# Kernel tuning notes

Measured on AMD Instinct MI355X. Metric: run time of the kernel, lower is better.

The kernel has to match this reference:

```python
import jax, jax.numpy as jnp
import numpy as np

INV_COEFF = 25.0
VAR_COEFF = 25.0
COV_COEFF = 1.0


def _cdist(a, b):
    # Euclidean pairwise distance, (B,N,C)x(B,M,C)->(B,N,M)
    a2 = jnp.sum(a * a, axis=-1)[:, :, None]
    b2 = jnp.sum(b * b, axis=-1)[:, None, :]
    d2 = a2 + b2 - 2.0 * jnp.einsum('bnc,bmc->bnm', a, b)
    return jnp.sqrt(jnp.maximum(d2, 0.0))


def _nn_match(input_maps, candidate_maps, distances, num_matches):
    # top-1 NN per input row, then keep the num_matches rows with the
    # smallest NN-distance, preserving original row order (matches the
    # torch sort/sort/mask + masked_select logic exactly).
    min_vals = jnp.min(distances, axis=-1)       # (B, N)
    nn_idx = jnp.argmin(distances, axis=-1)      # (B, N)
    order = jnp.argsort(min_vals, axis=1)[:, :num_matches]   # rows with smallest min-dist
    indices_selected = jnp.sort(order, axis=1)               # restore original order (B, M)
    nn_selected = jnp.take_along_axis(nn_idx, indices_selected, axis=1)  # (B, M)
    filt_in = jnp.take_along_axis(input_maps, indices_selected[..., None], axis=1)
    filt_cand = jnp.take_along_axis(candidate_maps, nn_selected[..., None], axis=1)
    return filt_in, filt_cand


def _vicreg_loss(x, y):
    # x, y: (B, M, C)
    B = x.shape[0]
    C = x.shape[-1]
    repr_loss = INV_COEFF * jnp.mean((x - y) ** 2)
    # gather_center: subtract batch mean (single-device equivalent)
    xc = x - jnp.mean(x, axis=0, keepdims=True)
    yc = y - jnp.mean(y, axis=0, keepdims=True)
    std_x = jnp.sqrt(jnp.var(xc, axis=0, ddof=1) + 1e-4)
    std_y = jnp.sqrt(jnp.var(yc, axis=0, ddof=1) + 1e-4)
    std_loss = VAR_COEFF * (jnp.mean(jax.nn.relu(1.0 - std_x)) / 2
                            + jnp.mean(jax.nn.relu(1.0 - std_y)) / 2)
    # covariance per location: permute to (M, B, C), center over batch
    xp = jnp.transpose(xc, (1, 0, 2))
    yp = jnp.transpose(yc, (1, 0, 2))
    xp = xp - jnp.mean(xp, axis=-2, keepdims=True)
    yp = yp - jnp.mean(yp, axis=-2, keepdims=True)
    cov_x = jnp.einsum('mnc,mnd->mcd', xp, xp) / (B - 1)
    cov_y = jnp.einsum('mnc,mnd->mcd', yp, yp) / (B - 1)
    off = 1.0 - jnp.eye(C, dtype=x.dtype)
    cov_loss = (jnp.sum((cov_x * off) ** 2, axis=(-2, -1)) / C / 2
                + jnp.sum((cov_y * off) ** 2, axis=(-2, -1)) / C / 2)
    cov_loss = COV_COEFF * jnp.mean(cov_loss)
    return repr_loss, std_loss, cov_loss


def _local_loss(maps_1, maps_2, location_1, location_2, num_matches):
    # L2-feature-space NN matching, both directions
    m1f_l2, m1nn_l2 = _nn_match(maps_1, maps_2, _cdist(maps_1, maps_2), num_matches)
    m2f_l2, m2nn_l2 = _nn_match(maps_2, maps_1, _cdist(maps_2, maps_1), num_matches)
    # location-space NN matching, both directions
    loc1 = location_1.reshape(location_1.shape[0], -1, location_1.shape[-1])
    loc2 = location_2.reshape(location_2.shape[0], -1, location_2.shape[-1])
    m1f_loc, m1nn_loc = _nn_match(maps_1, maps_2, _cdist(loc1, loc2), num_matches)
    m2f_loc, m2nn_loc = _nn_match(maps_2, maps_1, _cdist(loc2, loc1), num_matches)
    inv = var = cov = 0.0
    for a, b in ((m1f_l2, m1nn_l2), (m2f_l2, m2nn_l2),
                 (m1f_loc, m1nn_loc), (m2f_loc, m2nn_loc)):
        i, v, c = _vicreg_loss(a, b)
        inv = inv + i
        var = var + v
        cov = cov + c
    return inv + var + cov


def setup_inputs() -> dict:
    key = jax.random.key(0)
    k1, k2, k3, k4 = jax.random.split(key, 4)
    B, HW, C, H = 64, 784, 512, 28
    return {
        'maps_1': jax.random.normal(k1, (B, HW, C), dtype=jnp.float32),
        'maps_2': jax.random.normal(k2, (B, HW, C), dtype=jnp.float32),
        'location_1': jax.random.uniform(k3, (B, H, H, 2), dtype=jnp.float32),
        'location_2': jax.random.uniform(k4, (B, H, H, 2), dtype=jnp.float32),
        'num_matches': 256,
    }


def reference(maps_1, maps_2, location_1, location_2, num_matches):
    return _local_loss(maps_1, maps_2, location_1, location_2, num_matches)
```

## Files before the change

### kernel.cpp

```cpp
#include <hip/hip_runtime.h>
#include <stdint.h>

#define B 64
#define N 784
#define C 512
#define M 256

typedef unsigned long long u64;
typedef unsigned short u16;
typedef __attribute__((ext_vector_type(8))) short short8;
typedef __attribute__((ext_vector_type(4))) float f32x4;

static __device__ __forceinline__ u64 umin64(u64 a, u64 b) { return a < b ? a : b; }

static __device__ __forceinline__ u16 f2bf(float x) {
    unsigned u = __float_as_uint(x);
    return (u16)((u + 0x7FFFu + ((u >> 16) & 1u)) >> 16);
}
static __device__ __forceinline__ float b2f(u16 v) {
    return __uint_as_float((unsigned)v << 16);
}

static __device__ __forceinline__ void gload_lds16(const u16* g, u16* l) {
    __builtin_amdgcn_global_load_lds((const __attribute__((address_space(1))) void*)g,
                                     (__attribute__((address_space(3))) void*)l, 16, 0, 0);
}

__global__ __launch_bounds__(256) void convnorm_kernel(
    const float* __restrict__ m1, const float* __restrict__ m2,
    u16* __restrict__ abf, u16* __restrict__ bbf, float* __restrict__ nrm) {
    int w = blockIdx.x * 4 + (threadIdx.x >> 6);
    int lane = threadIdx.x & 63;
    if (w >= 2 * B * N) return;
    const float* src = (w < B * N) ? m1 : m2;
    u16* dst = (w < B * N) ? abf : bbf;
    int row = (w < B * N) ? w : w - B * N;
    const float4* p = (const float4*)(src + (size_t)row * C);
    u64* q = (u64*)(dst + (size_t)row * C);
    float s = 0.f;
#pragma unroll
    for (int i = 0; i < 2; ++i) {
        int idx = lane + i * 64;
        float4 v = p[idx];
        s += v.x * v.x + v.y * v.y + v.z * v.z + v.w * v.w;
        q[idx] = (u64)f2bf(v.x) | ((u64)f2bf(v.y) << 16) |
                 ((u64)f2bf(v.z) << 32) | ((u64)f2bf(v.w) << 48);
    }
#pragma unroll
    for (int off = 32; off > 0; off >>= 1) s += __shfl_down(s, off, 64);
    if (lane == 0) nrm[w] = s;
}

__global__ __launch_bounds__(256, 2) void feat_mfma_kernel(
    const u16* __restrict__ abf, const u16* __restrict__ bbf,
    const float* __restrict__ nrm, u64* __restrict__ rowkey) {
    int id = blockIdx.x;
    int xcd = id & 7;
    int q = id >> 3;
    int hi = q / 49, t49 = q - hi * 49;
    int b = hi * 8 + xcd;
    int tn = t49 / 7, tm = t49 - tn * 7;

    const int t = threadIdx.x;
    const int lane = t & 63, wv = t >> 6;
    const int wr = wv >> 1, wc = wv & 1;

    __shared__ __align__(16) u16 SM[2][2][128 * 64];
    __shared__ float sNa[128], sNb[128];

    const int row0 = tn * 128, col0 = tm * 128;
    if (t < 128) {
        int n = row0 + t;
        sNa[t] = (n < N) ? nrm[b * N + n] : __builtin_inff();
    } else {
        int m = col0 + (t - 128);
        sNb[t - 128] = (m < N) ? nrm[B * N + b * N + m] : __builtin_inff();
    }

    size_t aofs[4], bofs[4];
    int ldso[4];
#pragma unroll
    for (int s = 0; s < 4; ++s) {
        int c = (wv * 4 + s) * 64 + lane;
        int rl = c >> 3;
        int grp = (c & 7) ^ (rl & 7);
        int ga = row0 + rl; if (ga > N - 1) ga = N - 1;
        int gb = col0 + rl; if (gb > N - 1) gb = N - 1;
        aofs[s] = ((size_t)b * N + ga) * C + grp * 8;
        bofs[s] = ((size_t)b * N + gb) * C + grp * 8;
        ldso[s] = (wv * 4 + s) * 512;
    }

    f32x4 acc[4][4];
#pragma unroll
    for (int i = 0; i < 4; ++i)
#pragma unroll
        for (int j = 0; j < 4; ++j) acc[i][j] = (f32x4){0.f, 0.f, 0.f, 0.f};

#pragma unroll
    for (int s = 0; s < 4; ++s) {
        gload_lds16(abf + aofs[s], &SM[0][0][ldso[s]]);
        gload_lds16(bbf + bofs[s], &SM[0][1][ldso[s]]);
    }
    __syncthreads();

    for (int kt = 0; kt < 8; ++kt) {
        const int cur = kt & 1;
        if (kt < 7) {
            int ke = (kt + 1) * 64;
#pragma unroll
            for (int s = 0; s < 4; ++s) {
                gload_lds16(abf + aofs[s] + ke, &SM[cur ^ 1][0][ldso[s]]);
                gload_lds16(bbf + bofs[s] + ke, &SM[cur ^ 1][1][ldso[s]]);
            }
        }
        const u16* Als = SM[cur][0];
        const u16* Bls = SM[cur][1];
#pragma unroll
        for (int ks = 0; ks < 2; ++ks) {
            short8 afr[4], bfr[4];
            int cb = ks * 4 + (lane >> 4);
#pragma unroll
            for (int f = 0; f < 4; ++f) {
                int ra = wr * 64 + f * 16 + (lane & 15);
                afr[f] = *(const short8*)&Als[ra * 64 + ((cb ^ (ra & 7)) << 3)];
                int rb = wc * 64 + f * 16 + (lane & 15);
                bfr[f] = *(const short8*)&Bls[rb * 64 + ((cb ^ (rb & 7)) << 3)];
            }
#pragma unroll
            for (int fi = 0; fi < 4; ++fi)
#pragma unroll
                for (int fj = 0; fj < 4; ++fj)
                    acc[fi][fj] = __builtin_amdgcn_mfma_f32_16x16x32_bf16(
                        afr[fi], bfr[fj], acc[fi][fj], 0, 0, 0);
        }
        __syncthreads();
    }

    const int g4 = (lane >> 4) << 2;
    float na4[4][4], nb4[4];
#pragma unroll
    for (int fi = 0; fi < 4; ++fi) {
        float4 v = *(const float4*)&sNa[wr * 64 + fi * 16 + g4];
        na4[fi][0] = v.x; na4[fi][1] = v.y; na4[fi][2] = v.z; na4[fi][3] = v.w;
    }
#pragma unroll
    for (int fj = 0; fj < 4; ++fj) nb4[fj] = sNb[wc * 64 + fj * 16 + (lane & 15)];

    u64(*red)[33] = (u64(*)[33])SM;
    u64 ck[4] = {~0ull, ~0ull, ~0ull, ~0ull};
#pragma unroll
    for (int fi = 0; fi < 4; ++fi) {
        int rl = wr * 64 + fi * 16 + g4;
        u64 rk[4] = {~0ull, ~0ull, ~0ull, ~0ull};
#pragma unroll
        for (int fj = 0; fj < 4; ++fj) {
            unsigned colidx = (unsigned)(col0 + wc * 64 + fj * 16 + (lane & 15));
#pragma unroll
            for (int reg = 0; reg < 4; ++reg) {
                float d2 = fmaxf(na4[fi][reg] + nb4[fj] - 2.f * acc[fi][fj][reg], 0.f);
                u64 hv = ((u64)__float_as_uint(d2) << 32);
                rk[reg] = umin64(rk[reg], hv | colidx);
                ck[fj] = umin64(ck[fj], hv | (unsigned)(row0 + rl + reg));
            }
        }
#pragma unroll
        for (int reg = 0; reg < 4; ++reg)
            red[rl + reg][(wc << 4) | (lane & 15)] = rk[reg];
    }
#pragma unroll
    for (int fj = 0; fj < 4; ++fj) {
        u64 best = ck[fj];
        best = umin64(best, __shfl_xor(best, 16, 64));
        best = umin64(best, __shfl_xor(best, 32, 64));
        if (lane < 16) {
            int m = col0 + wc * 64 + fj * 16 + lane;
            if (m < N) atomicMin(&rowkey[(size_t)B * N + (size_t)b * N + m], best);
        }
    }
    __syncthreads();
    if (t < 128) {
        u64 best = red[t][0];
#pragma unroll
        for (int x = 1; x < 32; ++x) best = umin64(best, red[t][x]);
        int n = row0 + t;
        if (n < N) atomicMin(&rowkey[(size_t)b * N + n], best);
    }
}

__global__ __launch_bounds__(256) void loc_dist_kernel(
    const float* __restrict__ l1, const float* __restrict__ l2,
    u64* __restrict__ rowkey) {
    const int dir = blockIdx.z;
    const int b = blockIdx.y;
    const int t = threadIdx.x;
    const int n = blockIdx.x * 256 + t;
    __shared__ __align__(16) float4 s4[N];
    const float* Ap = dir ? l2 : l1;
    const float* Bp = dir ? l1 : l2;
    for (int i = t; i < N; i += 256) {
        float2 qv = ((const float2*)Bp)[b * N + i];
        s4[i] = make_float4(qv.x, qv.y, qv.x * qv.x + qv.y * qv.y, 0.f);
    }
    __syncthreads();
    if (n >= N) return;
    float2 a = ((const float2*)Ap)[b * N + n];
    float a2 = a.x * a.x + a.y * a.y;
    float nax = -2.f * a.x, nay = -2.f * a.y;
    u64 best = ~0ull;
#pragma unroll 4
    for (int mm = 0; mm < N; ++mm) {
        float4 v = s4[mm];
        float d2 = fmaxf(fmaf(nax, v.x, fmaf(nay, v.y, a2 + v.z)), 0.f);
        u64 kv = ((u64)__float_as_uint(d2) << 32) | (unsigned)mm;
        best = kv < best ? kv : best;
    }
    rowkey[(size_t)(2 + dir) * B * N + (size_t)b * N + n] = best;
}

__global__ __launch_bounds__(256) void select_kernel(
    const u64* __restrict__ rowkey, int* __restrict__ sel_idx,
    int* __restrict__ nn_idx) {
    const int b = blockIdx.x;
    const int dir = blockIdx.y;
    const int t = threadIdx.x;
    __shared__ u64 sk[1024];
    const u64* rk = rowkey + (size_t)dir * B * N + (size_t)b * N;
    for (int i = t; i < 1024; i += 256)
        sk[i] = (i < N) ? ((rk[i] & 0xFFFFFFFF00000000ull) | (unsigned)i) : ~0ull;
    __syncthreads();
    for (unsigned k = 2; k <= 1024; k <<= 1) {
        for (unsigned j = k >> 1; j > 0; j >>= 1) {
            for (unsigned i = t; i < 1024; i += 256) {
                unsigned ixj = i ^ j;
                if (ixj > i) {
                    u64 x = sk[i], y = sk[ixj];
                    bool up = ((i & k) == 0);
                    if ((x > y) == up) { sk[i] = y; sk[ixj] = x; }
                }
            }
            __syncthreads();
        }
    }
    unsigned myidx = (unsigned)(sk[t] & 0xFFFFFFFFull);
    __syncthreads();
    unsigned* si = (unsigned*)sk;
    si[t] = myidx;
    __syncthreads();
    for (unsigned k = 2; k <= 256; k <<= 1) {
        for (unsigned j = k >> 1; j > 0; j >>= 1) {
            unsigned i = t, ixj = i ^ j;
            if (ixj > i) {
                unsigned x = si[i], y = si[ixj];
                bool up = ((i & k) == 0);
                if ((x > y) == up) { si[i] = y; si[ixj] = x; }
            }
            __syncthreads();
        }
    }
    int sel = (int)si[t];
    sel_idx[((size_t)dir * B + b) * M + t] = sel;
    nn_idx[((size_t)dir * B + b) * M + t] = (int)(unsigned)(rk[sel] & 0xFFFFFFFFull);
}

__global__ __launch_bounds__(256, 2) void vicreg_mfma_kernel(
    const u16* __restrict__ abf, const u16* __restrict__ bbf,
    const int* __restrict__ sel_idx, const int* __restrict__ nn_idx,
    float* __restrict__ acc) {
    const int mloc = blockIdx.x;
    const int p = blockIdx.y;
    const int t = threadIdx.x;
    const int l = t & 63, w = t >> 6;

    __shared__ __align__(16) u16 Xs[2][64 * 128];
    __shared__ __align__(16) u16 Ys[2][64 * 128];
    __shared__ float colpart[4][4][128];
    __shared__ float Rsx[64], Rsy[64];
    __shared__ int xi[64], yi[64];
    __shared__ float redsc[4][4];

    if (t < 64) xi[t] = sel_idx[((size_t)p * B + t) * M + mloc];
    else if (t < 128) yi[t - 64] = nn_idx[((size_t)p * B + (t - 64)) * M + mloc];
    __syncthreads();

    const u16* Xg = (p & 1) ? bbf : abf;
    const u16* Yg = (p & 1) ? abf : bbf;
    unsigned xofs[4], yofs[4];
    int ldst[4];
#pragma unroll
    for (int s = 0; s < 4; ++s) {
        int r = w * 16 + s * 4 + (l >> 4);
        int cs = (l & 15) ^ (r & 15);
        xofs[s] = (unsigned)((r * N + xi[r]) * C + cs * 8);
        yofs[s] = (unsigned)((r * N + yi[r]) * C + cs * 8);
        ldst[s] = (w * 16 + s * 4) * 128;
    }

    f32x4 Gx[4], Gy[4], Z;
#pragma unroll
    for (int j = 0; j < 4; ++j) { Gx[j] = (f32x4){0,0,0,0}; Gy[j] = (f32x4){0,0,0,0}; }
    Z = (f32x4){0, 0, 0, 0};
    float stdacc = 0.f, covdacc = 0.f, reprp = 0.f;

#pragma unroll
    for (int s = 0; s < 4; ++s) {
        gload_lds16(Xg + xofs[s], &Xs[0][ldst[s]]);
        gload_lds16(Yg + yofs[s], &Ys[0][ldst[s]]);
    }
    __syncthreads();

    for (int kc = 0; kc < 4; ++kc) {
        const int cur = kc & 1;
        if (kc < 3) {
            int ke = (kc + 1) * 128;
#pragma unroll
            for (int s = 0; s < 4; ++s) {
                gload_lds16(Xg + xofs[s] + ke, &Xs[cur ^ 1][ldst[s]]);
                gload_lds16(Yg + yofs[s] + ke, &Ys[cur ^ 1][ldst[s]]);
            }
        }
        const u16* Xc = Xs[cur];
        const u16* Yc = Ys[cur];

#pragma unroll
        for (int ks = 0; ks < 4; ++ks) {
            int cb = ks * 4 + (l >> 4);
            int pe = (cb ^ (l & 15)) << 3;
            short8 ax = *(const short8*)&Xc[((w << 4) + (l & 15)) * 128 + pe];
            short8 ay = *(const short8*)&Yc[((w << 4) + (l & 15)) * 128 + pe];
            short8 bx[4], by[4];
#pragma unroll
            for (int j = 0; j < 4; ++j) {
                bx[j] = *(const short8*)&Xc[(j * 16 + (l & 15)) * 128 + pe];
                by[j] = *(const short8*)&Yc[(j * 16 + (l & 15)) * 128 + pe];
            }
#pragma unroll
            for (int j = 0; j < 4; ++j) {
                Gx[j] = __builtin_amdgcn_mfma_f32_16x16x32_bf16(ax, bx[j], Gx[j], 0, 0, 0);
                Gy[j] = __builtin_amdgcn_mfma_f32_16x16x32_bf16(ay, by[j], Gy[j], 0, 0, 0);
            }
            Z = __builtin_amdgcn_mfma_f32_16x16x32_bf16(ax, ay, Z, 0, 0, 0);
        }

        {
            int c4 = (l & 31) << 2;
            int cc = c4 >> 3, h = (c4 >> 2) & 1;
            int g2 = (w << 1) + (l >> 5);
            float s1x0 = 0, s1x1 = 0, s1x2 = 0, s1x3 = 0;
            float s2x0 = 0, s2x1 = 0, s2x2 = 0, s2x3 = 0;
            float s1y0 = 0, s1y1 = 0, s1y2 = 0, s1y3 = 0;
            float s2y0 = 0, s2y1 = 0, s2y2 = 0, s2y3 = 0;
#pragma unroll
            for (int rr = 0; rr < 8; ++rr) {
                int r = g2 * 8 + rr;
                int off = r * 128 + ((cc ^ (r & 15)) << 3) + h * 4;
                ushort4 vx = *(const ushort4*)&Xc[off];
                ushort4 vy = *(const ushort4*)&Yc[off];
                float x0 = b2f(vx.x), x1 = b2f(vx.y), x2 = b2f(vx.z), x3 = b2f(vx.w);
                float y0 = b2f(vy.x), y1 = b2f(vy.y), y2 = b2f(vy.z), y3 = b2f(vy.w);
                s1x0 += x0; s1x1 += x1; s1x2 += x2; s1x3 += x3;
                s2x0 = fmaf(x0, x0, s2x0); s2x1 = fmaf(x1, x1, s2x1);
                s2x2 = fmaf(x2, x2, s2x2); s2x3 = fmaf(x3, x3, s2x3);
                s1y0 += y0; s1y1 += y1; s1y2 += y2; s1y3 += y3;
                s2y0 = fmaf(y0, y0, s2y0); s2y1 = fmaf(y1, y1, s2y1);
                s2y2 = fmaf(y2, y2, s2y2); s2y3 = fmaf(y3, y3, s2y3);
            }
            s1x0 += __shfl_xor(s1x0, 32, 64); s1x1 += __shfl_xor(s1x1, 32, 64);
            s1x2 += __shfl_xor(s1x2, 32, 64); s1x3 += __shfl_xor(s1x3, 32, 64);
            s2x0 += __shfl_xor(s2x0, 32, 64); s2x1 += __shfl_xor(s2x1, 32, 64);
            s2x2 += __shfl_xor(s2x2, 32, 64); s2x3 += __shfl_xor(s2x3, 32, 64);
            s1y0 += __shfl_xor(s1y0, 32, 64); s1y1 += __shfl_xor(s1y1, 32, 64);
            s1y2 += __shfl_xor(s1y2, 32, 64); s1y3 += __shfl_xor(s1y3, 32, 64);
            s2y0 += __shfl_xor(s2y0, 32, 64); s2y1 += __shfl_xor(s2y1, 32, 64);
            s2y2 += __shfl_xor(s2y2, 32, 64); s2y3 += __shfl_xor(s2y3, 32, 64);
            if (l < 32) {
                *(float4*)&colpart[w][0][c4] = make_float4(s1x0, s1x1, s1x2, s1x3);
                *(float4*)&colpart[w][1][c4] = make_float4(s2x0, s2x1, s2x2, s2x3);
                *(float4*)&colpart[w][2][c4] = make_float4(s1y0, s1y1, s1y2, s1y3);
                *(float4*)&colpart[w][3][c4] = make_float4(s2y0, s2y1, s2y2, s2y3);
            }
        }
        __syncthreads();

        if (t < 128) {
            float s1x = 0, s2x = 0, s1y = 0, s2y = 0;
#pragma unroll
            for (int ww = 0; ww < 4; ++ww) {
                s1x += colpart[ww][0][t]; s2x += colpart[ww][1][t];
                s1y += colpart[ww][2][t]; s2y += colpart[ww][3][t];
            }
            float sx = s2x - s1x * s1x * (1.f / 64.f);
            float sy = s2y - s1y * s1y * (1.f / 64.f);
            stdacc += fmaxf(0.f, 1.f - sqrtf(sx * (1.f / 63.f) + 1e-4f)) +
                      fmaxf(0.f, 1.f - sqrtf(sy * (1.f / 63.f) + 1e-4f));
            covdacc += sx * sx + sy * sy;
            reprp += s2x + s2y;
        }
        __syncthreads();
    }

    float zd = 0.f;
    {
        int rbase = (l >> 4) << 2, col = l & 15;
#pragma unroll
        for (int reg = 0; reg < 4; ++reg)
            zd += (col == rbase + reg) ? Z[reg] : 0.f;
    }
    float rsx[4], rsy[4];
#pragma unroll
    for (int reg = 0; reg < 4; ++reg) {
        rsx[reg] = Gx[0][reg] + Gx[1][reg] + Gx[2][reg] + Gx[3][reg];
        rsy[reg] = Gy[0][reg] + Gy[1][reg] + Gy[2][reg] + Gy[3][reg];
    }
#pragma unroll
    for (int off = 1; off < 16; off <<= 1)
#pragma unroll
        for (int reg = 0; reg < 4; ++reg) {
            rsx[reg] += __shfl_xor(rsx[reg], off, 64);
            rsy[reg] += __shfl_xor(rsy[reg], off, 64);
        }
    if ((l & 15) == 0) {
#pragma unroll
        for (int reg = 0; reg < 4; ++reg) {
            Rsx[(w << 4) + ((l >> 4) << 2) + reg] = rsx[reg];
            Rsy[(w << 4) + ((l >> 4) << 2) + reg] = rsy[reg];
        }
    }
    __syncthreads();
    float myx = Rsx[l], myy = Rsy[l];
#pragma unroll
    for (int off = 1; off < 64; off <<= 1) {
        myx += __shfl_xor(myx, off, 64);
        myy += __shfl_xor(myy, off, 64);
    }
    float tX = myx * (1.f / 4096.f), tY = myy * (1.f / 4096.f);
    float kn = 0.f;
#pragma unroll
    for (int j = 0; j < 4; ++j) {
        float cX = Rsx[(j << 4) + (l & 15)] * (1.f / 64.f);
        float cY = Rsy[(j << 4) + (l & 15)] * (1.f / 64.f);
#pragma unroll
        for (int reg = 0; reg < 4; ++reg) {
            float K1 = Gx[j][reg] - rsx[reg] * (1.f / 64.f) - cX + tX;
            kn = fmaf(K1, K1, kn);
            float K2 = Gy[j][reg] - rsy[reg] * (1.f / 64.f) - cY + tY;
            kn = fmaf(K2, K2, kn);
        }
    }

    float v0 = reprp - 2.f * zd, v1 = stdacc, v2 = covdacc, v3 = kn;
#pragma unroll
    for (int off = 1; off < 64; off <<= 1) {
        v0 += __shfl_xor(v0, off, 64);
        v1 += __shfl_xor(v1, off, 64);
        v2 += __shfl_xor(v2, off, 64);
        v3 += __shfl_xor(v3, off, 64);
    }
    if (l == 0) { redsc[w][0] = v0; redsc[w][1] = v1; redsc[w][2] = v2; redsc[w][3] = v3; }
    __syncthreads();
    if (t == 0) {
        float r0 = 0, r1 = 0, r2 = 0, r3 = 0;
#pragma unroll
        for (int ww = 0; ww < 4; ++ww) {
            r0 += redsc[ww][0]; r1 += redsc[ww][1];
            r2 += redsc[ww][2]; r3 += redsc[ww][3];
        }
        atomicAdd(&acc[0], r0);
        atomicAdd(&acc[1], r1);
        atomicAdd(&acc[2], r3 - r2);
    }
}

__global__ __launch_bounds__(256) void norms_kernel(const float* __restrict__ m1,
                                                    const float* __restrict__ m2,
                                                    float* __restrict__ nrm) {
    int w = blockIdx.x * 4 + (threadIdx.x >> 6);
    int lane = threadIdx.x & 63;
    if (w >= 2 * B * N) return;
    const float* src = (w < B * N) ? m1 : m2;
    int row = (w < B * N) ? w : w - B * N;
    const float4* p = (const float4*)(src + (size_t)row * C);
    float s = 0.f;
#pragma unroll
    for (int i = 0; i < 2; ++i) {
        float4 v = p[lane + i * 64];
        s += v.x * v.x + v.y * v.y + v.z * v.z + v.w * v.w;
    }
#pragma unroll
    for (int off = 32; off > 0; off >>= 1) s += __shfl_down(s, off, 64);
    if (lane == 0) nrm[w] = s;
}

__global__ __launch_bounds__(256) void feat_dist_kernel(
    const float* __restrict__ m1, const float* __restrict__ m2,
    const float* __restrict__ nrm, u64* __restrict__ rowkey) {
    const int b = blockIdx.z;
    const int tn = blockIdx.x, tm = blockIdx.y;
    __shared__ float As[64][68];
    __shared__ float Bt[64][68];
    __shared__ u64 red[64][16];
    const int t = threadIdx.x;
    const int ty = t >> 4, tx = t & 15;
    float acc[4][4] = {};
    const float* A = m1 + (size_t)b * N * C;
    const float* Bm = m2 + (size_t)b * N * C;

    for (int k0 = 0; k0 < C; k0 += 64) {
#pragma unroll
        for (int it = 0; it < 4; ++it) {
            int idx = t + it * 256;
            int r = idx >> 4, cc = (idx & 15) << 2;
            int n = tn * 64 + r;
            float4 v = make_float4(0.f, 0.f, 0.f, 0.f);
            if (n < N) v = *(const float4*)(A + (size_t)n * C + k0 + cc);
            *(float4*)&As[r][cc] = v;
            int mm = tm * 64 + r;
            float4 w = make_float4(0.f, 0.f, 0.f, 0.f);
            if (mm < N) w = *(const float4*)(Bm + (size_t)mm * C + k0 + cc);
            Bt[cc + 0][r] = w.x; Bt[cc + 1][r] = w.y;
            Bt[cc + 2][r] = w.z; Bt[cc + 3][r] = w.w;
        }
        __syncthreads();
#pragma unroll 4
        for (int kq = 0; kq < 64; kq += 4) {
            float aa[4][4], bb[4][4];
#pragma unroll
            for (int i = 0; i < 4; ++i) {
                float4 v = *(const float4*)&As[ty * 4 + i][kq];
                aa[i][0] = v.x; aa[i][1] = v.y; aa[i][2] = v.z; aa[i][3] = v.w;
            }
#pragma unroll
            for (int qq = 0; qq < 4; ++qq) {
                float4 v = *(const float4*)&Bt[kq + qq][tx * 4];
                bb[qq][0] = v.x; bb[qq][1] = v.y; bb[qq][2] = v.z; bb[qq][3] = v.w;
            }
#pragma unroll
            for (int qq = 0; qq < 4; ++qq)
#pragma unroll
                for (int i = 0; i < 4; ++i)
#pragma unroll
                    for (int j = 0; j < 4; ++j)
                        acc[i][j] = fmaf(aa[i][qq], bb[qq][j], acc[i][j]);
        }
        __syncthreads();
    }

    u64 rk[4] = {~0ull, ~0ull, ~0ull, ~0ull};
    u64 ck[4] = {~0ull, ~0ull, ~0ull, ~0ull};
    const float* nr1 = nrm;
    const float* nr2 = nrm + B * N;
#pragma unroll
    for (int i = 0; i < 4; ++i) {
        int n = tn * 64 + ty * 4 + i;
        if (n >= N) continue;
        float a2 = nr1[b * N + n];
#pragma unroll
        for (int j = 0; j < 4; ++j) {
            int mm = tm * 64 + tx * 4 + j;
            if (mm >= N) continue;
            float b2 = nr2[b * N + mm];
            float d2 = a2 + b2 - 2.f * acc[i][j];
            unsigned vb = __float_as_uint(fmaxf(d2, 0.f));
            u64 kv = ((u64)vb << 32);
            rk[i] = umin64(rk[i], kv | (unsigned)mm);
            ck[j] = umin64(ck[j], kv | (unsigned)n);
        }
    }
#pragma unroll
    for (int i = 0; i < 4; ++i) red[ty * 4 + i][tx] = rk[i];
    __syncthreads();
    if (t < 64) {
        u64 best = red[t][0];
#pragma unroll
        for (int x = 1; x < 16; ++x) best = umin64(best, red[t][x]);
        int n = tn * 64 + t;
        if (n < N && best != ~0ull)
            atomicMin(&rowkey[(size_t)b * N + n], best);
    }
    __syncthreads();
#pragma unroll
    for (int j = 0; j < 4; ++j) red[tx * 4 + j][ty] = ck[j];
    __syncthreads();
    if (t < 64) {
        u64 best = red[t][0];
#pragma unroll
        for (int x = 1; x < 16; ++x) best = umin64(best, red[t][x]);
        int mm = tm * 64 + t;
        if (mm < N && best != ~0ull)
            atomicMin(&rowkey[(size_t)B * N + (size_t)b * N + mm], best);
    }
}

__device__ __forceinline__ float blockReduce(float v, float* redb, int t) {
    __syncthreads();
    redb[t] = v;
    __syncthreads();
    for (int s = 128; s > 0; s >>= 1) {
        if (t < s) redb[t] += redb[t + s];
        __syncthreads();
    }
    return redb[0];
}

__global__ __launch_bounds__(256) void vicreg_kernel(
    const float* __restrict__ m1, const float* __restrict__ m2,
    const int* __restrict__ sel_idx, const int* __restrict__ nn_idx,
    float* __restrict__ acc) {
    const int mloc = blockIdx.x;
    const int p = blockIdx.y;
    const int t = threadIdx.x;
    const float* X = (p & 1) ? m2 : m1;
    const float* Y = (p & 1) ? m1 : m2;
    __shared__ float Xs[64][65];
    __shared__ float Ys[64][65];
    __shared__ int xi[64], yi[64];
    __shared__ float pst[192][5];
    __shared__ float Rs[64];
    __shared__ float Tsh;
    __shared__ float redb[256];

    if (t < 64) {
        xi[t] = sel_idx[((size_t)p * B + t) * M + mloc];
        yi[t] = nn_idx[((size_t)p * B + t) * M + mloc];
    }
    __syncthreads();

    float Gx[4][4] = {}, Gy[4][4] = {};
    float stdx = 0, stdy = 0, covdx = 0, covdy = 0, repr = 0;
    const int i0 = (t >> 4) << 2, j0 = (t & 15) << 2;

    for (int c0 = 0; c0 < C; c0 += 64) {
#pragma unroll
        for (int it = 0; it < 4; ++it) {
            int fidx = t + it * 256;
            int r = fidx >> 4, cc = (fidx & 15) << 2;
            float4 v = *(const float4*)(X + ((size_t)r * N + xi[r]) * C + c0 + cc);
            Xs[r][cc] = v.x; Xs[r][cc + 1] = v.y; Xs[r][cc + 2] = v.z; Xs[r][cc + 3] = v.w;
            float4 w = *(const float4*)(Y + ((size_t)r * N + yi[r]) * C + c0 + cc);
            Ys[r][cc] = w.x; Ys[r][cc + 1] = w.y; Ys[r][cc + 2] = w.z; Ys[r][cc + 3] = w.w;
        }
        __syncthreads();
#pragma unroll 4
        for (int k = 0; k < 64; ++k) {
            float ax[4], bx[4], ay[4], by[4];
#pragma unroll
            for (int i = 0; i < 4; ++i) { ax[i] = Xs[i0 + i][k]; ay[i] = Ys[i0 + i][k]; }
#pragma unroll
            for (int j = 0; j < 4; ++j) { bx[j] = Xs[j0 + j][k]; by[j] = Ys[j0 + j][k]; }
#pragma unroll
            for (int i = 0; i < 4; ++i)
#pragma unroll
                for (int j = 0; j < 4; ++j) {
                    Gx[i][j] = fmaf(ax[i], bx[j], Gx[i][j]);
                    Gy[i][j] = fmaf(ay[i], by[j], Gy[i][j]);
                }
        }
        {
            float s1x = 0, s2x = 0, s1y = 0, s2y = 0, sxy = 0;
            int col = t & 63, g = t >> 6;
            for (int r = g * 16; r < g * 16 + 16; ++r) {
                float xv = Xs[r][col], yv = Ys[r][col];
                s1x += xv; s2x += xv * xv;
                s1y += yv; s2y += yv * yv;
                sxy += xv * yv;
            }
            if (g) {
                float* qq = pst[(g - 1) * 64 + col];
                qq[0] = s1x; qq[1] = s2x; qq[2] = s1y; qq[3] = s2y; qq[4] = sxy;
            }
            __syncthreads();
            if (g == 0) {
#pragma unroll
                for (int gg = 0; gg < 3; ++gg) {
                    float* qq = pst[gg * 64 + col];
                    s1x += qq[0]; s2x += qq[1]; s1y += qq[2]; s2y += qq[3]; sxy += qq[4];
                }
                float xb = s1x * (1.f / 64.f);
                float sx = s2x - 64.f * xb * xb;
                float yb = s1y * (1.f / 64.f);
                float sy = s2y - 64.f * yb * yb;
                stdx += fmaxf(0.f, 1.f - sqrtf(sx * (1.f / 63.f) + 1e-4f));
                stdy += fmaxf(0.f, 1.f - sqrtf(sy * (1.f / 63.f) + 1e-4f));
                covdx += sx * sx;
                covdy += sy * sy;
                repr += s2x + s2y - 2.f * sxy;
            }
            __syncthreads();
        }
    }

    float knx = 0.f, kny = 0.f;
    float (*Gs)[65] = (float(*)[65]) & Xs[0][0];
    __syncthreads();
#pragma unroll
    for (int i = 0; i < 4; ++i)
#pragma unroll
        for (int j = 0; j < 4; ++j) Gs[i0 + i][j0 + j] = Gx[i][j];
    __syncthreads();
    if (t < 64) {
        float r = 0;
        for (int j = 0; j < 64; ++j) r += Gs[t][j];
        Rs[t] = r;
    }
    __syncthreads();
    if (t < 64) {
        float r = Rs[t];
#pragma unroll
        for (int off = 32; off > 0; off >>= 1) r += __shfl_down(r, off, 64);
        if (t == 0) Tsh = r;
    }
    __syncthreads();
    {
        float T = Tsh * (1.f / 4096.f);
#pragma unroll
        for (int i = 0; i < 4; ++i)
#pragma unroll
            for (int j = 0; j < 4; ++j) {
                float Kij = Gx[i][j] - (Rs[i0 + i] + Rs[j0 + j]) * (1.f / 64.f) + T;
                knx = fmaf(Kij, Kij, knx);
            }
    }
    __syncthreads();
#pragma unroll
    for (int i = 0; i < 4; ++i)
#pragma unroll
        for (int j = 0; j < 4; ++j) Gs[i0 + i][j0 + j] = Gy[i][j];
    __syncthreads();
    if (t < 64) {
        float r = 0;
        for (int j = 0; j < 64; ++j) r += Gs[t][j];
        Rs[t] = r;
    }
    __syncthreads();
    if (t < 64) {
        float r = Rs[t];
#pragma unroll
        for (int off = 32; off > 0; off >>= 1) r += __shfl_down(r, off, 64);
        if (t == 0) Tsh = r;
    }
    __syncthreads();
    {
        float T = Tsh * (1.f / 4096.f);
#pragma unroll
        for (int i = 0; i < 4; ++i)
#pragma unroll
            for (int j = 0; j < 4; ++j) {
                float Kij = Gy[i][j] - (Rs[i0 + i] + Rs[j0 + j]) * (1.f / 64.f) + T;
                kny = fmaf(Kij, Kij, kny);
            }
    }

    float v_repr = blockReduce(repr, redb, t);
    float v_std = blockReduce(stdx + stdy, redb, t);
    float v_covd = blockReduce(covdx + covdy, redb, t);
    float v_kn = blockReduce(knx + kny, redb, t);
    if (t == 0) {
        atomicAdd(&acc[0], v_repr);
        atomicAdd(&acc[1], v_std);
        atomicAdd(&acc[2], v_kn - v_covd);
    }
}

__global__ void finalize_kernel(const float* __restrict__ acc, float* __restrict__ out) {
    if (threadIdx.x == 0 && blockIdx.x == 0) {
        float repr = 25.f * acc[0] / ((float)B * (float)M * (float)C);
        float stdl = 12.5f * acc[1] / ((float)M * (float)C);
        float cov = acc[2] / (63.f * 63.f * (float)C * 2.f) / (float)M;
        out[0] = repr + stdl + cov;
    }
}

extern "C" void kernel_launch(void* const* d_in, const int* in_sizes, int n_in,
                              void* d_out, int out_size, void* d_ws, size_t ws_size,
                              hipStream_t stream) {
    const float* m1 = (const float*)d_in[0];
    const float* m2 = (const float*)d_in[1];
    const float* l1 = (const float*)d_in[2];
    const float* l2 = (const float*)d_in[3];
    float* out = (float*)d_out;
    char* ws = (char*)d_ws;

    u64* rowkey = (u64*)ws;
    size_t off = (size_t)4 * B * N * sizeof(u64);
    float* nrm = (float*)(ws + off); off += (size_t)2 * B * N * sizeof(float);
    int* sel_idx = (int*)(ws + off); off += (size_t)4 * B * M * sizeof(int);
    int* nn_idx = (int*)(ws + off);  off += (size_t)4 * B * M * sizeof(int);
    float* acc = (float*)(ws + off); off += 256;
    off = (off + 255) & ~(size_t)255;
    u16* abf = (u16*)(ws + off);
    u16* bbf = abf + (size_t)B * N * C;
    size_t need = off + (size_t)2 * B * N * C * sizeof(u16);
    bool use_mfma = ws_size >= need;

    hipMemsetAsync(rowkey, 0xFF, (size_t)4 * B * N * sizeof(u64), stream);
    hipMemsetAsync(acc, 0, 32, stream);
    if (use_mfma) {
        convnorm_kernel<<<dim3(2 * B * N / 4), dim3(256), 0, stream>>>(m1, m2, abf, bbf, nrm);
        feat_mfma_kernel<<<dim3(64 * 49), dim3(256), 0, stream>>>(abf, bbf, nrm, rowkey);
    } else {
        norms_kernel<<<dim3(2 * B * N / 4), dim3(256), 0, stream>>>(m1, m2, nrm);
        feat_dist_kernel<<<dim3(13, 13, B), dim3(256), 0, stream>>>(m1, m2, nrm, rowkey);
    }
    loc_dist_kernel<<<dim3((N + 255) / 256, B, 2), dim3(256), 0, stream>>>(l1, l2, rowkey);
    select_kernel<<<dim3(B, 4), dim3(256), 0, stream>>>(rowkey, sel_idx, nn_idx);
    if (use_mfma) {
        vicreg_mfma_kernel<<<dim3(M, 4), dim3(256), 0, stream>>>(abf, bbf, sel_idx, nn_idx, acc);
    } else {
        vicreg_kernel<<<dim3(M, 4), dim3(256), 0, stream>>>(m1, m2, sel_idx, nn_idx, acc);
    }
    finalize_kernel<<<dim3(1), dim3(64), 0, stream>>>(acc, out);
}
```

Baseline: 264.8 us.

## Prefetch all vicreg chunks upfront, double-buffer colpart, fold memsets into kernels

The vicreg MFMA kernel now issues all four K-chunk gathers into LDS at the start instead of double-buffering one chunk ahead. It also double-buffers the column-partial scratch so one barrier per iteration can be dropped. The acc zeroing moves into select_kernel and the rowkey memset shrinks to the half that loc_dist does not overwrite, removing launch overhead. The cost is twice the LDS use, which drops occupancy to one block per CU per launch bounds.

After: 263.8 us. About the same (-0.4%).

```diff
diff --git a/kernel.cpp b/kernel.cpp
--- a/kernel.cpp
+++ b/kernel.cpp
@@ -220,10 +220,11 @@
 
 __global__ __launch_bounds__(256) void select_kernel(
     const u64* __restrict__ rowkey, int* __restrict__ sel_idx,
-    int* __restrict__ nn_idx) {
+    int* __restrict__ nn_idx, float* __restrict__ acc) {
     const int b = blockIdx.x;
     const int dir = blockIdx.y;
     const int t = threadIdx.x;
+    if (b == 0 && dir == 0 && t < 8) acc[t] = 0.f;
     __shared__ u64 sk[1024];
     const u64* rk = rowkey + (size_t)dir * B * N + (size_t)b * N;
     for (int i = t; i < 1024; i += 256)
@@ -263,7 +264,7 @@
     nn_idx[((size_t)dir * B + b) * M + t] = (int)(unsigned)(rk[sel] & 0xFFFFFFFFull);
 }
 
-__global__ __launch_bounds__(256, 2) void vicreg_mfma_kernel(
+__global__ __launch_bounds__(256, 1) void vicreg_mfma_kernel(
     const u16* __restrict__ abf, const u16* __restrict__ bbf,
     const int* __restrict__ sel_idx, const int* __restrict__ nn_idx,
     float* __restrict__ acc) {
@@ -272,9 +273,9 @@
     const int t = threadIdx.x;
     const int l = t & 63, w = t >> 6;
 
-    __shared__ __align__(16) u16 Xs[2][64 * 128];
-    __shared__ __align__(16) u16 Ys[2][64 * 128];
-    __shared__ float colpart[4][4][128];
+    __shared__ __align__(16) u16 Xs[4][64 * 128];
+    __shared__ __align__(16) u16 Ys[4][64 * 128];
+    __shared__ float colpart[2][4][4][128];
     __shared__ float Rsx[64], Rsy[64];
     __shared__ int xi[64], yi[64];
     __shared__ float redsc[4][4];
@@ -296,6 +297,15 @@
         ldst[s] = (w * 16 + s * 4) * 128;
     }
 
+#pragma unroll
+    for (int kc = 0; kc < 4; ++kc)
+#pragma unroll
+        for (int s = 0; s < 4; ++s) {
+            gload_lds16(Xg + xofs[s] + kc * 128, &Xs[kc][ldst[s]]);
+            gload_lds16(Yg + yofs[s] + kc * 128, &Ys[kc][ldst[s]]);
+        }
+    __syncthreads();
+
     f32x4 Gx[4], Gy[4], Z;
 #pragma unroll
     for (int j = 0; j < 4; ++j) { Gx[j] = (f32x4){0,0,0,0}; Gy[j] = (f32x4){0,0,0,0}; }
@@ -303,24 +313,9 @@
     float stdacc = 0.f, covdacc = 0.f, reprp = 0.f;
 
 #pragma unroll
-    for (int s = 0; s < 4; ++s) {
-        gload_lds16(Xg + xofs[s], &Xs[0][ldst[s]]);
-        gload_lds16(Yg + yofs[s], &Ys[0][ldst[s]]);
-    }
-    __syncthreads();
-
     for (int kc = 0; kc < 4; ++kc) {
-        const int cur = kc & 1;
-        if (kc < 3) {
-            int ke = (kc + 1) * 128;
-#pragma unroll
-            for (int s = 0; s < 4; ++s) {
-                gload_lds16(Xg + xofs[s] + ke, &Xs[cur ^ 1][ldst[s]]);
-                gload_lds16(Yg + yofs[s] + ke, &Ys[cur ^ 1][ldst[s]]);
-            }
-        }
-        const u16* Xc = Xs[cur];
-        const u16* Yc = Ys[cur];
+        const u16* Xc = Xs[kc];
+        const u16* Yc = Ys[kc];
 
 #pragma unroll
         for (int ks = 0; ks < 4; ++ks) {
@@ -374,10 +369,10 @@
             s2y0 += __shfl_xor(s2y0, 32, 64); s2y1 += __shfl_xor(s2y1, 32, 64);
             s2y2 += __shfl_xor(s2y2, 32, 64); s2y3 += __shfl_xor(s2y3, 32, 64);
             if (l < 32) {
-                *(float4*)&colpart[w][0][c4] = make_float4(s1x0, s1x1, s1x2, s1x3);
-                *(float4*)&colpart[w][1][c4] = make_float4(s2x0, s2x1, s2x2, s2x3);
-                *(float4*)&colpart[w][2][c4] = make_float4(s1y0, s1y1, s1y2, s1y3);
-                *(float4*)&colpart[w][3][c4] = make_float4(s2y0, s2y1, s2y2, s2y3);
+                *(float4*)&colpart[kc & 1][w][0][c4] = make_float4(s1x0, s1x1, s1x2, s1x3);
+                *(float4*)&colpart[kc & 1][w][1][c4] = make_float4(s2x0, s2x1, s2x2, s2x3);
+                *(float4*)&colpart[kc & 1][w][2][c4] = make_float4(s1y0, s1y1, s1y2, s1y3);
+                *(float4*)&colpart[kc & 1][w][3][c4] = make_float4(s2y0, s2y1, s2y2, s2y3);
             }
         }
         __syncthreads();
@@ -386,8 +381,8 @@
             float s1x = 0, s2x = 0, s1y = 0, s2y = 0;
 #pragma unroll
             for (int ww = 0; ww < 4; ++ww) {
-                s1x += colpart[ww][0][t]; s2x += colpart[ww][1][t];
-                s1y += colpart[ww][2][t]; s2y += colpart[ww][3][t];
+                s1x += colpart[kc & 1][ww][0][t]; s2x += colpart[kc & 1][ww][1][t];
+                s1y += colpart[kc & 1][ww][2][t]; s2y += colpart[kc & 1][ww][3][t];
             }
             float sx = s2x - s1x * s1x * (1.f / 64.f);
             float sy = s2y - s1y * s1y * (1.f / 64.f);
@@ -396,7 +391,6 @@
             covdacc += sx * sx + sy * sy;
             reprp += s2x + s2y;
         }
-        __syncthreads();
     }
 
     float zd = 0.f;
@@ -792,8 +786,7 @@
     size_t need = off + (size_t)2 * B * N * C * sizeof(u16);
     bool use_mfma = ws_size >= need;
 
-    hipMemsetAsync(rowkey, 0xFF, (size_t)4 * B * N * sizeof(u64), stream);
-    hipMemsetAsync(acc, 0, 32, stream);
+    hipMemsetAsync(rowkey, 0xFF, (size_t)2 * B * N * sizeof(u64), stream);
     if (use_mfma) {
         convnorm_kernel<<<dim3(2 * B * N / 4), dim3(256), 0, stream>>>(m1, m2, abf, bbf, nrm);
         feat_mfma_kernel<<<dim3(64 * 49), dim3(256), 0, stream>>>(abf, bbf, nrm, rowkey);
@@ -802,7 +795,7 @@
         feat_dist_kernel<<<dim3(13, 13, B), dim3(256), 0, stream>>>(m1, m2, nrm, rowkey);
     }
     loc_dist_kernel<<<dim3((N + 255) / 256, B, 2), dim3(256), 0, stream>>>(l1, l2, rowkey);
-    select_kernel<<<dim3(B, 4), dim3(256), 0, stream>>>(rowkey, sel_idx, nn_idx);
+    select_kernel<<<dim3(B, 4), dim3(256), 0, stream>>>(rowkey, sel_idx, nn_idx, acc);
     if (use_mfma) {
         vicreg_mfma_kernel<<<dim3(M, 4), dim3(256), 0, stream>>>(abf, bbf, sel_idx, nn_idx, acc);
     } else {
```
